# Performance work log

Hardware: AMD Instinct MI355X
Metric: run time of the kernel (lower is better)

The kernel has to match this reference:

```python
import jax, jax.numpy as jnp
import numpy as np

NUM_CLASS = 5
IN_SIZE = 4
OBS_LEN = 20
EMBED = 256
B = 2048
N = 64
NUM_MODES = 20
IN_DIM = IN_SIZE * OBS_LEN  # 80


def setup_inputs() -> dict:
    key = jax.random.key(0)
    ks = jax.random.split(key, 12)
    s = 1.0 / np.sqrt(IN_DIM)
    inp = {
        "obs": jax.random.normal(ks[0], (B, OBS_LEN, IN_SIZE), jnp.float32),
        "neis": jax.random.normal(ks[1], (B, N, OBS_LEN, IN_SIZE), jnp.float32),
        "self_labels": jax.random.randint(ks[2], (B,), 0, NUM_CLASS),
        "nei_labels": jax.random.randint(ks[3], (B, N), 0, NUM_CLASS + 1),
        "modes": jax.random.normal(ks[4], (NUM_CLASS, NUM_MODES, EMBED), jnp.float32),
        # per-class obs embedding (ModuleList of Linear(in_dim, embed))
        "obs_W": jax.random.uniform(ks[5], (NUM_CLASS, IN_DIM, EMBED), jnp.float32, -s, s),
        "obs_b": jax.random.uniform(ks[6], (NUM_CLASS, EMBED), jnp.float32, -s, s),
        # per-class neighbor embedding (num_class+1 Linears)
        "nei_W": jax.random.uniform(ks[7], (NUM_CLASS + 1, IN_DIM, EMBED), jnp.float32, -s, s),
        "nei_b": jax.random.uniform(ks[8], (NUM_CLASS + 1, EMBED), jnp.float32, -s, s),
        # mode embedding Linear(2*embed, embed)
        "mode_W": jax.random.uniform(ks[9], (2 * EMBED, EMBED), jnp.float32, -1.0 / np.sqrt(2 * EMBED), 1.0 / np.sqrt(2 * EMBED)),
        "mode_b": jax.random.uniform(ks[10], (EMBED,), jnp.float32, -1.0 / np.sqrt(2 * EMBED), 1.0 / np.sqrt(2 * EMBED)),
    }
    return inp


def reference(obs, neis, self_labels, nei_labels, modes, obs_W, obs_b, nei_W, nei_b, mode_W, mode_b):
    obs_f = obs.reshape(B, IN_DIM)            # [B, in_dim]
    neis_f = neis.reshape(B, N, IN_DIM)       # [B, N, in_dim]
    eps = jnp.float32(1e-4)

    # label-routed obs embedding: one-hot selects the per-class Linear
    oh_s = jax.nn.one_hot(self_labels, NUM_CLASS, dtype=obs.dtype)          # [B, C]
    x = jnp.einsum("bi,cio,bc->bo", obs_f, obs_W, oh_s) + obs_b[self_labels]  # [B, E]

    # elementwise reciprocal transform (class-independent, applied to every neighbor row)
    r = jnp.where(neis_f >= 0, 1.0 / (neis_f + eps), 1.0 / (neis_f - eps))   # [B, N, in_dim]

    # label-routed neighbor embedding over num_class+1 experts
    oh_n = jax.nn.one_hot(nei_labels, NUM_CLASS + 1, dtype=obs.dtype)        # [B, N, C+1]
    nei_feats = jnp.einsum("bni,cio,bnc->bno", r, nei_W, oh_n) + nei_b[nei_labels]  # [B, N, E]

    mode_feats = modes[self_labels]                                          # [B, M, E]
    x_tiled = jnp.broadcast_to(x[:, None, :], (B, NUM_MODES, EMBED))
    cat = jnp.concatenate([x_tiled, mode_feats], axis=-1)                    # [B, M, 2E]
    out = jnp.einsum("bmk,ko->bmo", cat, mode_W) + mode_b                    # [B, M, E]
    return (out, nei_feats)
```

## Files before the change

kernel.cpp:

```cpp
#include <hip/hip_runtime.h>

#define BATCH 2048
#define NNEI 64
#define IN_DIM 80
#define EMBED 256
#define NCLS 5
#define NMODES 20
#define NROWS (BATCH * NNEI)
#define NEXP (NCLS + 1)
#define TM 16
#define GRID2 512
#define MAXT 104

#define NBIN (NROWS / 256)
#define NWF 144
#define NPRJ (NCLS * NMODES)

typedef __attribute__((ext_vector_type(8))) short bf16x8;
typedef __attribute__((ext_vector_type(4))) float f32x4;
typedef __attribute__((ext_vector_type(4))) int i32x4;

__device__ inline unsigned short bf16_rne(float f) {
    unsigned u = __builtin_bit_cast(unsigned, f);
    unsigned r = (u + 0x7fffu + ((u >> 16) & 1u)) >> 16;
    return (unsigned short)r;
}
__device__ inline float bf16_to_f(unsigned short h) {
    unsigned u = ((unsigned)h) << 16;
    return __builtin_bit_cast(float, u);
}
__device__ inline void st_nt(float* p, float v) { __builtin_nontemporal_store(v, p); }

__global__ void prep_all(const int* __restrict__ nei_labels,
                         int* __restrict__ counts, int* __restrict__ lists,
                         const float* __restrict__ nei_W, unsigned short* __restrict__ wfrag,
                         const float* __restrict__ modes, const float* __restrict__ mode_W,
                         const float* __restrict__ mode_b, float* __restrict__ proj) {
    __shared__ int lc[NEXP], lb[NEXP];
    const int b = blockIdx.x;
    const int t = threadIdx.x;

    if (b < NBIN) {
        if (t < NEXP) lc[t] = 0;
        __syncthreads();
        int r = b * 256 + t;
        int c = nei_labels[r];
        int lpos = atomicAdd(&lc[c], 1);
        __syncthreads();
        if (t < NEXP) lb[t] = atomicAdd(&counts[t], lc[t]);
        __syncthreads();
        lists[(size_t)c * NROWS + lb[c] + lpos] = r;
    } else if (b < NBIN + NWF) {
        int e = (b - NBIN) * 4 + (t >> 6);
        int l = t & 63;
        int part = e & 1;
        int cfg = (e >> 1) & 15;
        int ks = (e >> 5) % 3;
        int c = e / 96;
        int col = cfg * 16 + (l & 15);
        unsigned short v[8] __attribute__((aligned(16)));
        #pragma unroll
        for (int j = 0; j < 8; ++j) {
            int k = ks * 32 + ((l >> 4) * 8) + j;
            float w = (k < IN_DIM) ? nei_W[((size_t)c * IN_DIM + k) * EMBED + col] : 0.f;
            unsigned short h = bf16_rne(w);
            if (part == 0) v[j] = h;
            else v[j] = bf16_rne(w - bf16_to_f(h));
        }
        unsigned short* dst = wfrag + ((size_t)e * 64 + l) * 8;
        *reinterpret_cast<i32x4*>(dst) = *reinterpret_cast<const i32x4*>(v);
    } else {
        int cm = b - (NBIN + NWF);
        int o = t;
        const float* mv = modes + (size_t)cm * EMBED;
        float acc = mode_b[o];
        #pragma unroll 8
        for (int k = 0; k < EMBED; ++k)
            acc = fmaf(mv[k], mode_W[(size_t)(EMBED + k) * EMBED + o], acc);
        proj[(size_t)cm * EMBED + o] = acc;
    }
}

#define BPB 2
__global__ __launch_bounds__(256, 4)
void obs_mode(const float* __restrict__ obs, const int* __restrict__ self_labels,
              const float* __restrict__ obs_W, const float* __restrict__ obs_b,
              const float* __restrict__ mode_W, const float* __restrict__ proj,
              float* __restrict__ out0) {
    int b0 = blockIdx.x * BPB;
    int o = threadIdx.x;
    __shared__ float obs_s[BPB][IN_DIM];
    __shared__ float x_s[BPB][EMBED];
    __shared__ int cls_s[BPB];

    for (int t = threadIdx.x; t < BPB * IN_DIM; t += 256) {
        int bb = t / IN_DIM, k = t % IN_DIM;
        obs_s[bb][k] = obs[(size_t)(b0 + bb) * IN_DIM + k];
    }
    if (threadIdx.x < BPB) cls_s[threadIdx.x] = self_labels[b0 + threadIdx.x];
    __syncthreads();

    int c[BPB];
    float xacc[BPB];
    #pragma unroll
    for (int bb = 0; bb < BPB; ++bb) {
        c[bb] = cls_s[bb];
        xacc[bb] = obs_b[c[bb] * EMBED + o];
    }
    #pragma unroll 4
    for (int k = 0; k < IN_DIM; ++k) {
        #pragma unroll
        for (int bb = 0; bb < BPB; ++bb)
            xacc[bb] = fmaf(obs_s[bb][k],
                            obs_W[(size_t)c[bb] * IN_DIM * EMBED + (size_t)k * EMBED + o],
                            xacc[bb]);
    }
    #pragma unroll
    for (int bb = 0; bb < BPB; ++bb) x_s[bb][o] = xacc[bb];
    __syncthreads();

    float tacc[BPB];
    #pragma unroll
    for (int bb = 0; bb < BPB; ++bb) tacc[bb] = 0.f;
    #pragma unroll 4
    for (int k = 0; k < EMBED; ++k) {
        float wv = mode_W[(size_t)k * EMBED + o];
        #pragma unroll
        for (int bb = 0; bb < BPB; ++bb)
            tacc[bb] = fmaf(x_s[bb][k], wv, tacc[bb]);
    }
    #pragma unroll
    for (int bb = 0; bb < BPB; ++bb) {
        const float* pj = proj + (size_t)c[bb] * NMODES * EMBED;
        float* op = out0 + (size_t)(b0 + bb) * NMODES * EMBED;
        for (int m = 0; m < NMODES; ++m)
            st_nt(&op[m * EMBED + o], tacc[bb] + pj[m * EMBED + o]);
    }
}

__global__ __launch_bounds__(256, 2)
void nei_gemv_mfma(const float* __restrict__ neis,
                   const unsigned short* __restrict__ wfrag,
                   const float* __restrict__ nei_b,
                   const int* __restrict__ counts,
                   const int* __restrict__ lists,
                   float* __restrict__ out_n) {
    const int b = blockIdx.x;
    const int c = (b * NEXP) / GRID2;
    const int cstart = (c * GRID2 + NEXP - 1) / NEXP;
    const int cend = ((c + 1) * GRID2 + NEXP - 1) / NEXP;
    const int blk = b - cstart;
    const int nblk = cend - cstart;
    const int cnt = counts[c];
    const int ntiles = (cnt + TM - 1) / TM;

    __shared__ int rids_s[MAXT * TM];

    if (blk >= ntiles || cnt == 0) return;
    const int nt = min((ntiles - blk + nblk - 1) / nblk, MAXT);

    const int ch = threadIdx.x >> 6;
    const int l = threadIdx.x & 63;
    const int* mylist = lists + (size_t)c * NROWS;
    const int kc = (l >> 4) * 8;

    for (int i = threadIdx.x; i < nt * TM; i += 256) {
        int j = i >> 4, r = i & 15;
        int gi = (blk + j * nblk) * TM + r;
        rids_s[i] = mylist[min(gi, cnt - 1)];
    }

    bf16x8 wh[3][4], wl[3][4];
    {
        const unsigned short* wb = wfrag + (size_t)c * 96 * 64 * 8;
        #pragma unroll
        for (int ks = 0; ks < 3; ++ks)
            #pragma unroll
            for (int cf = 0; cf < 4; ++cf) {
                size_t base = ((((size_t)ks * 16 + (ch * 4 + cf)) * 2) * 64 + l) * 8;
                wh[ks][cf] = *reinterpret_cast<const bf16x8*>(wb + base);
                wl[ks][cf] = *reinterpret_cast<const bf16x8*>(wb + base + 64 * 8);
            }
    }
    #pragma unroll
    for (int ks = 0; ks < 3; ++ks)
        #pragma unroll
        for (int cf = 0; cf < 4; ++cf) {
            i32x4 th = __builtin_bit_cast(i32x4, wh[ks][cf]);
            asm volatile("" : "+v"(th));
            wh[ks][cf] = __builtin_bit_cast(bf16x8, th);
            i32x4 tl = __builtin_bit_cast(i32x4, wl[ks][cf]);
            asm volatile("" : "+v"(tl));
            wl[ks][cf] = __builtin_bit_cast(bf16x8, tl);
        }
    float bias[4];
    #pragma unroll
    for (int cf = 0; cf < 4; ++cf) {
        bias[cf] = nei_b[c * EMBED + (ch * 4 + cf) * 16 + (l & 15)];
        asm volatile("" : "+v"(bias[cf]));
    }
    __syncthreads();

#define LOADJ(F, R, J) {                                                      \
    R = rids_s[(J) * TM + (l & 15)];                                          \
    const float* bp_ = neis + (size_t)(unsigned)R * IN_DIM;                   \
    _Pragma("unroll")                                                         \
    for (int ks_ = 0; ks_ < 3; ++ks_) {                                       \
        int k0_ = ks_ * 32 + kc;                                              \
        if (k0_ + 8 > IN_DIM) k0_ = 0;          \
        *reinterpret_cast<float4*>(&F[ks_ * 8])     = *reinterpret_cast<const float4*>(bp_ + k0_);     \
        *reinterpret_cast<float4*>(&F[ks_ * 8 + 4]) = *reinterpret_cast<const float4*>(bp_ + k0_ + 4); \
    } }

#define COMPJ(F, R, J) {                                                      \
    bf16x8 ah_[3], al_[3];                                                    \
    _Pragma("unroll")                                                         \
    for (int ks_ = 0; ks_ < 3; ++ks_) {                                       \
        _Pragma("unroll")                                                     \
        for (int j_ = 0; j_ < 8; ++j_) {                                      \
            float v_ = F[ks_ * 8 + j_];                                       \
            float d_ = (v_ >= 0.f) ? (v_ + 1e-4f) : (v_ - 1e-4f);             \
            float r_ = __builtin_amdgcn_rcpf(d_);                             \
            unsigned short hi_ = bf16_rne(r_);                                \
            ah_[ks_][j_] = (short)hi_;                                        \
            al_[ks_][j_] = (short)bf16_rne(r_ - bf16_to_f(hi_));              \
        }                                                                     \
    }                                                                         \
    f32x4 acc_[4];                                                            \
    _Pragma("unroll")                                                         \
    for (int cf_ = 0; cf_ < 4; ++cf_) acc_[cf_] = (f32x4){0.f, 0.f, 0.f, 0.f};\
    _Pragma("unroll")                                                         \
    for (int ks_ = 0; ks_ < 3; ++ks_) {                                       \
        _Pragma("unroll")                                                     \
        for (int cf_ = 0; cf_ < 4; ++cf_) {                                   \
            acc_[cf_] = __builtin_amdgcn_mfma_f32_16x16x32_bf16(ah_[ks_], wh[ks_][cf_], acc_[cf_], 0, 0, 0); \
            acc_[cf_] = __builtin_amdgcn_mfma_f32_16x16x32_bf16(al_[ks_], wh[ks_][cf_], acc_[cf_], 0, 0, 0); \
            acc_[cf_] = __builtin_amdgcn_mfma_f32_16x16x32_bf16(ah_[ks_], wl[ks_][cf_], acc_[cf_], 0, 0, 0); \
        }                                                                     \
    }                                                                         \
    int rb_ = (l >> 4) * 4;                                                   \
    int tbase_ = (blk + (J) * nblk) * TM;                                     \
    _Pragma("unroll")                                                         \
    for (int i_ = 0; i_ < 4; ++i_) {                                          \
        int rid_ = __shfl(R, rb_ + i_);                                       \
        if (tbase_ + rb_ + i_ < cnt) {                                        \
            float* op_ = out_n + (size_t)(unsigned)rid_ * EMBED + (l & 15);   \
            _Pragma("unroll")                                                 \
            for (int cf_ = 0; cf_ < 4; ++cf_)                                 \
                st_nt(&op_[(ch * 4 + cf_) * 16], acc_[cf_][i_] + bias[cf_]);  \
        }                                                                     \
    } }

    float fA[24], fB[24], fC[24];
    int ridA, ridB, ridC;
    LOADJ(fA, ridA, 0)
    if (nt > 1) LOADJ(fB, ridB, 1)
    int j = 0;
    while (true) {
        if (j + 2 < nt) LOADJ(fC, ridC, j + 2)
        COMPJ(fA, ridA, j)
        if (j + 1 >= nt) break;
        if (j + 3 < nt) LOADJ(fA, ridA, j + 3)
        COMPJ(fB, ridB, j + 1)
        if (j + 2 >= nt) break;
        if (j + 4 < nt) LOADJ(fB, ridB, j + 4)
        COMPJ(fC, ridC, j + 2)
        if (j + 3 >= nt) break;
        j += 3;
    }
#undef LOADJ
#undef COMPJ
}

extern "C" void kernel_launch(void* const* d_in, const int* in_sizes, int n_in,
                              void* d_out, int out_size, void* d_ws, size_t ws_size,
                              hipStream_t stream) {
    const float* obs         = (const float*)d_in[0];
    const float* neis        = (const float*)d_in[1];
    const int*   self_labels = (const int*)d_in[2];
    const int*   nei_labels  = (const int*)d_in[3];
    const float* modes       = (const float*)d_in[4];
    const float* obs_W       = (const float*)d_in[5];
    const float* obs_b       = (const float*)d_in[6];
    const float* nei_W       = (const float*)d_in[7];
    const float* nei_b       = (const float*)d_in[8];
    const float* mode_W      = (const float*)d_in[9];
    const float* mode_b      = (const float*)d_in[10];

    float* out0  = (float*)d_out;
    float* out_n = out0 + (size_t)BATCH * NMODES * EMBED;

    char* ws = (char*)d_ws;
    int* counts = (int*)ws;
    int* lists  = (int*)(ws + 256);
    float* proj = (float*)(ws + 256 + (size_t)NEXP * NROWS * 4);
    unsigned short* wfrag = (unsigned short*)(ws + 256 + (size_t)NEXP * NROWS * 4
                                              + (size_t)NCLS * NMODES * EMBED * 4);

    hipMemsetAsync(counts, 0, NEXP * sizeof(int), stream);

    prep_all<<<NBIN + NWF + NPRJ, 256, 0, stream>>>(nei_labels, counts, lists,
                                                    nei_W, wfrag,
                                                    modes, mode_W, mode_b, proj);
    obs_mode<<<BATCH / BPB, 256, 0, stream>>>(obs, self_labels, obs_W, obs_b,
                                              mode_W, proj, out0);
    nei_gemv_mfma<<<GRID2, 256, 0, stream>>>(neis, wfrag, nei_b,
                                             counts, lists, out_n);
}
```

Baseline: 96.16 us.

## Stage reciprocal-packed neighbor tiles in LDS and split obs_mode to one row per block

The neighbor kernel no longer has every wavefront load and convert the same 16x80 tile redundantly. All 256 threads now cooperatively load the tile once, apply the reciprocal and bf16 hi/lo split, and write it into a double-buffered LDS area that the MFMA waves read, with block barriers between tiles. This removes the 4x duplicated global loads and reciprocal math per tile, at the cost of LDS traffic and a __syncthreads per tile in place of the earlier three-deep register prefetch. Separately, obs_mode goes from two batch rows per block to one, doubling the grid and raising the occupancy hint.

Measured after the change: 100.4 us. +4.4%, slower.

```diff
diff --git a/kernel.cpp b/kernel.cpp
--- a/kernel.cpp
+++ b/kernel.cpp
@@ -19,6 +19,7 @@
 typedef __attribute__((ext_vector_type(8))) short bf16x8;
 typedef __attribute__((ext_vector_type(4))) float f32x4;
 typedef __attribute__((ext_vector_type(4))) int i32x4;
+typedef __attribute__((ext_vector_type(2))) int i32x2;
 
 __device__ inline unsigned short bf16_rne(float f) {
     unsigned u = __builtin_bit_cast(unsigned, f);
@@ -30,6 +31,18 @@
     return __builtin_bit_cast(float, u);
 }
 __device__ inline void st_nt(float* p, float v) { __builtin_nontemporal_store(v, p); }
+
+__device__ inline void pack4(float4 v, unsigned short* hv, unsigned short* lv) {
+    float vv[4] = {v.x, v.y, v.z, v.w};
+    #pragma unroll
+    for (int j = 0; j < 4; ++j) {
+        float d = (vv[j] >= 0.f) ? (vv[j] + 1e-4f) : (vv[j] - 1e-4f);
+        float r = __builtin_amdgcn_rcpf(d);
+        unsigned short hi = bf16_rne(r);
+        hv[j] = hi;
+        lv[j] = bf16_rne(r - bf16_to_f(hi));
+    }
+}
 
 __global__ void prep_all(const int* __restrict__ nei_labels,
                          int* __restrict__ counts, int* __restrict__ lists,
@@ -81,61 +94,39 @@
     }
 }
 
-#define BPB 2
-__global__ __launch_bounds__(256, 4)
+__global__ __launch_bounds__(256, 8)
 void obs_mode(const float* __restrict__ obs, const int* __restrict__ self_labels,
               const float* __restrict__ obs_W, const float* __restrict__ obs_b,
               const float* __restrict__ mode_W, const float* __restrict__ proj,
               float* __restrict__ out0) {
-    int b0 = blockIdx.x * BPB;
+    int b = blockIdx.x;
     int o = threadIdx.x;
-    __shared__ float obs_s[BPB][IN_DIM];
-    __shared__ float x_s[BPB][EMBED];
-    __shared__ int cls_s[BPB];
-
-    for (int t = threadIdx.x; t < BPB * IN_DIM; t += 256) {
-        int bb = t / IN_DIM, k = t % IN_DIM;
-        obs_s[bb][k] = obs[(size_t)(b0 + bb) * IN_DIM + k];
-    }
-    if (threadIdx.x < BPB) cls_s[threadIdx.x] = self_labels[b0 + threadIdx.x];
+    __shared__ float obs_s[IN_DIM];
+    __shared__ float x_s[EMBED];
+    __shared__ int cls_s;
+
+    if (o < IN_DIM) obs_s[o] = obs[(size_t)b * IN_DIM + o];
+    if (o == 0) cls_s = self_labels[b];
     __syncthreads();
 
-    int c[BPB];
-    float xacc[BPB];
-    #pragma unroll
-    for (int bb = 0; bb < BPB; ++bb) {
-        c[bb] = cls_s[bb];
-        xacc[bb] = obs_b[c[bb] * EMBED + o];
-    }
+    int c = cls_s;
+    float xacc = obs_b[c * EMBED + o];
     #pragma unroll 4
-    for (int k = 0; k < IN_DIM; ++k) {
-        #pragma unroll
-        for (int bb = 0; bb < BPB; ++bb)
-            xacc[bb] = fmaf(obs_s[bb][k],
-                            obs_W[(size_t)c[bb] * IN_DIM * EMBED + (size_t)k * EMBED + o],
-                            xacc[bb]);
-    }
-    #pragma unroll
-    for (int bb = 0; bb < BPB; ++bb) x_s[bb][o] = xacc[bb];
+    for (int k = 0; k < IN_DIM; ++k)
+        xacc = fmaf(obs_s[k], obs_W[(size_t)c * IN_DIM * EMBED + (size_t)k * EMBED + o], xacc);
+    x_s[o] = xacc;
     __syncthreads();
 
-    float tacc[BPB];
-    #pragma unroll
-    for (int bb = 0; bb < BPB; ++bb) tacc[bb] = 0.f;
+    float tacc = 0.f;
     #pragma unroll 4
-    for (int k = 0; k < EMBED; ++k) {
-        float wv = mode_W[(size_t)k * EMBED + o];
-        #pragma unroll
-        for (int bb = 0; bb < BPB; ++bb)
-            tacc[bb] = fmaf(x_s[bb][k], wv, tacc[bb]);
-    }
-    #pragma unroll
-    for (int bb = 0; bb < BPB; ++bb) {
-        const float* pj = proj + (size_t)c[bb] * NMODES * EMBED;
-        float* op = out0 + (size_t)(b0 + bb) * NMODES * EMBED;
-        for (int m = 0; m < NMODES; ++m)
-            st_nt(&op[m * EMBED + o], tacc[bb] + pj[m * EMBED + o]);
-    }
+    for (int k = 0; k < EMBED; ++k)
+        tacc = fmaf(x_s[k], mode_W[(size_t)k * EMBED + o], tacc);
+
+    const float* pj = proj + (size_t)c * NMODES * EMBED;
+    float* op = out0 + (size_t)b * NMODES * EMBED;
+    #pragma unroll 4
+    for (int m = 0; m < NMODES; ++m)
+        st_nt(&op[m * EMBED + o], tacc + pj[m * EMBED + o]);
 }
 
 __global__ __launch_bounds__(256, 2)
@@ -155,19 +146,33 @@
     const int ntiles = (cnt + TM - 1) / TM;
 
     __shared__ int rids_s[MAXT * TM];
+    __shared__ __align__(16) unsigned short abuf[2][3072];
 
     if (blk >= ntiles || cnt == 0) return;
     const int nt = min((ntiles - blk + nblk - 1) / nblk, MAXT);
 
-    const int ch = threadIdx.x >> 6;
-    const int l = threadIdx.x & 63;
+    const int t = threadIdx.x;
+    const int ch = t >> 6;
+    const int l = t & 63;
     const int* mylist = lists + (size_t)c * NROWS;
-    const int kc = (l >> 4) * 8;
-
-    for (int i = threadIdx.x; i < nt * TM; i += 256) {
+
+    const int row0 = t / 20, qq0 = t - row0 * 20;
+    const int ks0 = qq0 >> 3, lg0 = (qq0 >> 1) & 3, hf0 = qq0 & 1;
+    const int off0 = ks0 * 1024 + (row0 + (lg0 << 4)) * 8 + hf0 * 4;
+    const int f1 = 256 + t;
+    const int row1 = f1 / 20, qq1 = f1 - row1 * 20;
+    const int ks1 = qq1 >> 3, lg1 = (qq1 >> 1) & 3, hf1 = qq1 & 1;
+    const int off1 = ks1 * 1024 + (row1 + (lg1 << 4)) * 8 + hf1 * 4;
+    const bool own1 = (t < 64);
+
+    for (int i = t; i < nt * TM; i += 256) {
         int j = i >> 4, r = i & 15;
         int gi = (blk + j * nblk) * TM + r;
         rids_s[i] = mylist[min(gi, cnt - 1)];
+    }
+    if (t < 128) {
+        int nb = t >> 6, part = (t >> 5) & 1, lane = 32 + (t & 31);
+        *reinterpret_cast<i32x4*>(&abuf[nb][2 * 1024 + part * 512 + lane * 8]) = (i32x4){0, 0, 0, 0};
     }
 
     bf16x8 wh[3][4], wl[3][4];
@@ -201,30 +206,36 @@
     }
     __syncthreads();
 
-#define LOADJ(F, R, J) {                                                      \
-    R = rids_s[(J) * TM + (l & 15)];                                          \
-    const float* bp_ = neis + (size_t)(unsigned)R * IN_DIM;                   \
-    _Pragma("unroll")                                                         \
-    for (int ks_ = 0; ks_ < 3; ++ks_) {                                       \
-        int k0_ = ks_ * 32 + kc;                                              \
-        if (k0_ + 8 > IN_DIM) k0_ = 0;          \
-        *reinterpret_cast<float4*>(&F[ks_ * 8])     = *reinterpret_cast<const float4*>(bp_ + k0_);     \
-        *reinterpret_cast<float4*>(&F[ks_ * 8 + 4]) = *reinterpret_cast<const float4*>(bp_ + k0_ + 4); \
+    float4 q0, q1;
+
+#define SISSUE(J) {                                                           \
+    int rid0_ = rids_s[(J) * TM + row0];                                      \
+    q0 = *reinterpret_cast<const float4*>(neis + (size_t)(unsigned)rid0_ * IN_DIM + qq0 * 4); \
+    if (own1) {                                                               \
+        int rid1_ = rids_s[(J) * TM + row1];                                  \
+        q1 = *reinterpret_cast<const float4*>(neis + (size_t)(unsigned)rid1_ * IN_DIM + qq1 * 4); \
     } }
 
-#define COMPJ(F, R, J) {                                                      \
+#define SPACK(NB) {                                                           \
+    unsigned short hv_[4] __attribute__((aligned(8)));                        \
+    unsigned short lv_[4] __attribute__((aligned(8)));                        \
+    pack4(q0, hv_, lv_);                                                      \
+    unsigned short* d0_ = &abuf[NB][off0];                                    \
+    *reinterpret_cast<i32x2*>(d0_)       = *reinterpret_cast<const i32x2*>(hv_); \
+    *reinterpret_cast<i32x2*>(d0_ + 512) = *reinterpret_cast<const i32x2*>(lv_); \
+    if (own1) {                                                               \
+        pack4(q1, hv_, lv_);                                                  \
+        unsigned short* d1_ = &abuf[NB][off1];                                \
+        *reinterpret_cast<i32x2*>(d1_)       = *reinterpret_cast<const i32x2*>(hv_); \
+        *reinterpret_cast<i32x2*>(d1_ + 512) = *reinterpret_cast<const i32x2*>(lv_); \
+    } }
+
+#define SCOMP(J, CB) {                                                        \
     bf16x8 ah_[3], al_[3];                                                    \
     _Pragma("unroll")                                                         \
     for (int ks_ = 0; ks_ < 3; ++ks_) {                                       \
-        _Pragma("unroll")                                                     \
-        for (int j_ = 0; j_ < 8; ++j_) {                                      \
-            float v_ = F[ks_ * 8 + j_];                                       \
-            float d_ = (v_ >= 0.f) ? (v_ + 1e-4f) : (v_ - 1e-4f);             \
-            float r_ = __builtin_amdgcn_rcpf(d_);                             \
-            unsigned short hi_ = bf16_rne(r_);                                \
-            ah_[ks_][j_] = (short)hi_;                                        \
-            al_[ks_][j_] = (short)bf16_rne(r_ - bf16_to_f(hi_));              \
-        }                                                                     \
+        ah_[ks_] = *reinterpret_cast<const bf16x8*>(&abuf[CB][ks_ * 1024 + l * 8]);       \
+        al_[ks_] = *reinterpret_cast<const bf16x8*>(&abuf[CB][ks_ * 1024 + 512 + l * 8]); \
     }                                                                         \
     f32x4 acc_[4];                                                            \
     _Pragma("unroll")                                                         \
@@ -242,7 +253,7 @@
     int tbase_ = (blk + (J) * nblk) * TM;                                     \
     _Pragma("unroll")                                                         \
     for (int i_ = 0; i_ < 4; ++i_) {                                          \
-        int rid_ = __shfl(R, rb_ + i_);                                       \
+        int rid_ = rids_s[(J) * TM + rb_ + i_];                               \
         if (tbase_ + rb_ + i_ < cnt) {                                        \
             float* op_ = out_n + (size_t)(unsigned)rid_ * EMBED + (l & 15);   \
             _Pragma("unroll")                                                 \
@@ -251,25 +262,22 @@
         }                                                                     \
     } }
 
-    float fA[24], fB[24], fC[24];
-    int ridA, ridB, ridC;
-    LOADJ(fA, ridA, 0)
-    if (nt > 1) LOADJ(fB, ridB, 1)
-    int j = 0;
-    while (true) {
-        if (j + 2 < nt) LOADJ(fC, ridC, j + 2)
-        COMPJ(fA, ridA, j)
-        if (j + 1 >= nt) break;
-        if (j + 3 < nt) LOADJ(fA, ridA, j + 3)
-        COMPJ(fB, ridB, j + 1)
-        if (j + 2 >= nt) break;
-        if (j + 4 < nt) LOADJ(fB, ridB, j + 4)
-        COMPJ(fC, ridC, j + 2)
-        if (j + 3 >= nt) break;
-        j += 3;
-    }
-#undef LOADJ
-#undef COMPJ
+    SISSUE(0)
+    SPACK(0)
+    __syncthreads();
+    int cb = 0;
+    for (int jt = 0; jt < nt; ++jt) {
+        bool hn = (jt + 1 < nt);
+        if (hn) SISSUE(jt + 1)
+        SCOMP(jt, cb)
+        if (!hn) break;
+        SPACK(cb ^ 1)
+        __syncthreads();
+        cb ^= 1;
+    }
+#undef SISSUE
+#undef SPACK
+#undef SCOMP
 }
 
 extern "C" void kernel_launch(void* const* d_in, const int* in_sizes, int n_in,
@@ -302,8 +310,8 @@
     prep_all<<<NBIN + NWF + NPRJ, 256, 0, stream>>>(nei_labels, counts, lists,
                                                     nei_W, wfrag,
                                                     modes, mode_W, mode_b, proj);
-    obs_mode<<<BATCH / BPB, 256, 0, stream>>>(obs, self_labels, obs_W, obs_b,
-                                              mode_W, proj, out0);
+    obs_mode<<<BATCH, 256, 0, stream>>>(obs, self_labels, obs_W, obs_b,
+                                        mode_W, proj, out0);
     nei_gemv_mfma<<<GRID2, 256, 0, stream>>>(neis, wfrag, nei_b,
                                              counts, lists, out_n);
 }
```
